# Performance work log

Hardware: AMD Instinct MI355X
Metric: run time of the kernel (lower is better)

The kernel has to match this reference:

```python
import jax, jax.numpy as jnp
import numpy as np

EPS = 1e-6
B = 4194304


def setup_inputs() -> dict:
    key = jax.random.key(0)
    k1, k2 = jax.random.split(key)
    ypred = jax.random.normal(k1, (B, 3, 3), dtype=jnp.float32)
    ytrue = jax.random.normal(k2, (B, 3, 3), dtype=jnp.float32)
    return {"ypred": ypred, "ytrue": ytrue}


def reference(ypred, ytrue):
    # trace(A^T B) == sum(A * B) elementwise -> one fused reduce per sample
    tr = jnp.sum(ypred * ytrue, axis=(1, 2))  # [B]
    cos = jnp.clip((tr - 1.0) * 0.5, -1.0 + EPS, 1.0 - EPS)
    angle = jnp.arccos(cos)
    return jnp.mean(angle)
```

## Files before the change

### kernel.cpp

```cpp
#include <hip/hip_runtime.h>


constexpr int TPB  = 256;
constexpr int NBLK = 2048;
constexpr float EPSF = 1e-6f;

__device__ __forceinline__ double block_reduce(double v) {
    __shared__ double sm[TPB / 64];
    const int lane = threadIdx.x & 63;
    const int wid  = threadIdx.x >> 6;
    #pragma unroll
    for (int off = 32; off > 0; off >>= 1) v += __shfl_down(v, off, 64);
    if (lane == 0) sm[wid] = v;
    __syncthreads();
    if (wid == 0) {
        v = (lane < TPB / 64) ? sm[lane] : 0.0;
        #pragma unroll
        for (int off = (TPB / 64) / 2; off > 0; off >>= 1) v += __shfl_down(v, off, 64);
    }
    return v;
}

__global__ __launch_bounds__(TPB) void geo_partial(
    const float* __restrict__ a, const float* __restrict__ b,
    double* __restrict__ partial, int nsamp)
{
    const long long tid    = (long long)blockIdx.x * TPB + threadIdx.x;
    const long long stride = (long long)gridDim.x * TPB;
    double acc = 0.0;

    for (long long g = tid; g * 4 < nsamp; g += stride) {
        const long long s0 = g * 4;
        const float4* pa = reinterpret_cast<const float4*>(a + s0 * 9);
        const float4* pb = reinterpret_cast<const float4*>(b + s0 * 9);

        float va[36], vb[36];
        #pragma unroll
        for (int j = 0; j < 9; ++j) {
            float4 x = pa[j];
            va[4*j+0] = x.x; va[4*j+1] = x.y; va[4*j+2] = x.z; va[4*j+3] = x.w;
        }
        #pragma unroll
        for (int j = 0; j < 9; ++j) {
            float4 y = pb[j];
            vb[4*j+0] = y.x; vb[4*j+1] = y.y; vb[4*j+2] = y.z; vb[4*j+3] = y.w;
        }

        #pragma unroll
        for (int k = 0; k < 4; ++k) {
            if (s0 + k < nsamp) {
                float dot = 0.0f;
                #pragma unroll
                for (int j = 0; j < 9; ++j) dot = fmaf(va[9*k+j], vb[9*k+j], dot);
                float c = (dot - 1.0f) * 0.5f;
                c = fminf(fmaxf(c, -1.0f + EPSF), 1.0f - EPSF);
                acc += (double)acosf(c);
            }
        }
    }

    double r = block_reduce(acc);
    if (threadIdx.x == 0) partial[blockIdx.x] = r;
}

__global__ __launch_bounds__(TPB) void geo_final(
    const double* __restrict__ partial, float* __restrict__ out,
    int n, double inv_n)
{
    double acc = 0.0;
    for (int i = threadIdx.x; i < n; i += TPB) acc += partial[i];
    double r = block_reduce(acc);
    if (threadIdx.x == 0) out[0] = (float)(r * inv_n);
}

extern "C" void kernel_launch(void* const* d_in, const int* in_sizes, int n_in,
                              void* d_out, int out_size, void* d_ws, size_t ws_size,
                              hipStream_t stream) {
    const float* a = (const float*)d_in[0];
    const float* b = (const float*)d_in[1];
    float* out = (float*)d_out;
    const int nsamp = in_sizes[0] / 9;

    double* partial = (double*)d_ws;

    geo_partial<<<NBLK, TPB, 0, stream>>>(a, b, partial, nsamp);
    geo_final<<<1, TPB, 0, stream>>>(partial, out, NBLK, 1.0 / (double)nsamp);
}
```

Before: 314.9 us.

## Load float4s coalesced per wave and assemble 3x3 dot products via lane shuffles

Each wave now reads 63 consecutive float4s from each input, covering 28 samples, so every lane does one coalesced load instead of nine strided float4 loads per thread. Each lane computes partial sums of its four products, and two cross-lane shuffles assemble each sample's 9-element dot product on an owner lane. This removes the uncoalesced access pattern and the large per-thread register arrays. The cost is extra shuffle and select logic, one idle lane per wave, and only 4 of 9 lanes computing acos, which lowers utilisation of the math units.

Result: faster. 308.6 us (-2.0%).

```diff
diff --git a/kernel.cpp b/kernel.cpp
--- a/kernel.cpp
+++ b/kernel.cpp
@@ -25,33 +25,46 @@
     const float* __restrict__ a, const float* __restrict__ b,
     double* __restrict__ partial, int nsamp)
 {
-    const long long tid    = (long long)blockIdx.x * TPB + threadIdx.x;
-    const long long stride = (long long)gridDim.x * TPB;
+    const int lane = threadIdx.x & 63;
+    const int wid  = threadIdx.x >> 6;
+    const long long gwave  = (long long)blockIdx.x * (TPB / 64) + wid;
+    const long long nwaves = (long long)gridDim.x * (TPB / 64);
+
+    const int g = lane / 9;
+    const int r = lane - 9 * g;
+    const bool active = (lane < 63);
+    const int head = (4 * r) / 9;
+    int nh = 9 * (head + 1) - 4 * r;
+    if (nh > 4) nh = 4;
+    const bool owner = active && ((r & 1) == 0) && (r < 8);
+    const int k = r >> 1;
+
+    const long long total_f4 = (long long)nsamp * 9 / 4;
+    const long long n_iters  = ((long long)nsamp + 27) / 28;
+
+    const float4* a4 = reinterpret_cast<const float4*>(a);
+    const float4* b4 = reinterpret_cast<const float4*>(b);
+
     double acc = 0.0;
+    for (long long it = gwave; it < n_iters; it += nwaves) {
+        const long long f4i = it * 63 + lane;
+        float4 x = make_float4(0.f, 0.f, 0.f, 0.f);
+        float4 y = make_float4(0.f, 0.f, 0.f, 0.f);
+        if (active && f4i < total_f4) { x = a4[f4i]; y = b4[f4i]; }
 
-    for (long long g = tid; g * 4 < nsamp; g += stride) {
-        const long long s0 = g * 4;
-        const float4* pa = reinterpret_cast<const float4*>(a + s0 * 9);
-        const float4* pb = reinterpret_cast<const float4*>(b + s0 * 9);
+        const float p0 = x.x * y.x, p1 = x.y * y.y, p2 = x.z * y.z, p3 = x.w * y.w;
+        const float pre2 = p0 + p1, pre3 = pre2 + p2, pre4 = pre3 + p3;
+        const float suf3 = p3, suf2 = p2 + p3, suf1 = p1 + suf2;
+        const float pearly = (nh == 1) ? p0 : (nh == 2) ? pre2 : (nh == 3) ? pre3 : pre4;
+        const float plate  = (nh == 4) ? pre4 : (nh == 1) ? suf1 : (nh == 2) ? suf2 : suf3;
 
-        float va[36], vb[36];
-        #pragma unroll
-        for (int j = 0; j < 9; ++j) {
-            float4 x = pa[j];
-            va[4*j+0] = x.x; va[4*j+1] = x.y; va[4*j+2] = x.z; va[4*j+3] = x.w;
-        }
-        #pragma unroll
-        for (int j = 0; j < 9; ++j) {
-            float4 y = pb[j];
-            vb[4*j+0] = y.x; vb[4*j+1] = y.y; vb[4*j+2] = y.z; vb[4*j+3] = y.w;
-        }
+        const float v1 = __shfl(plate,  lane + 1, 64);
+        const float v2 = __shfl(pearly, lane + 2, 64);
 
-        #pragma unroll
-        for (int k = 0; k < 4; ++k) {
-            if (s0 + k < nsamp) {
-                float dot = 0.0f;
-                #pragma unroll
-                for (int j = 0; j < 9; ++j) dot = fmaf(va[9*k+j], vb[9*k+j], dot);
+        if (owner) {
+            const long long s = it * 28 + 4 * g + k;
+            if (s < nsamp) {
+                const float dot = plate + v1 + v2;
                 float c = (dot - 1.0f) * 0.5f;
                 c = fminf(fmaxf(c, -1.0f + EPSF), 1.0f - EPSF);
                 acc += (double)acosf(c);
@@ -59,8 +72,8 @@
         }
     }
 
-    double r = block_reduce(acc);
-    if (threadIdx.x == 0) partial[blockIdx.x] = r;
+    const double rsum = block_reduce(acc);
+    if (threadIdx.x == 0) partial[blockIdx.x] = rsum;
 }
 
 __global__ __launch_bounds__(TPB) void geo_final(
@@ -69,7 +82,7 @@
 {
     double acc = 0.0;
     for (int i = threadIdx.x; i < n; i += TPB) acc += partial[i];
-    double r = block_reduce(acc);
+    const double r = block_reduce(acc);
     if (threadIdx.x == 0) out[0] = (float)(r * inv_n);
 }
 
```

## Stage sample tiles into LDS via double-buffered direct global-to-LDS loads

Applied to the files above, without the earlier changes.

Replaces per-thread strided float4 loads of 4 samples (144-byte stride, poorly coalesced) with wave-cooperative, fully coalesced global_load_lds transfers into double-buffered shared-memory tiles of 256 samples. Each thread then reads its 9 floats from LDS with an odd stride, which avoids bank conflicts. Manual vmcnt waits and barriers overlap the next tile's load with the current tile's compute. The grid is fixed at 1024 blocks × 16 tiles and has no grid-stride fallback, so it assumes the sample count is covered exactly.

Result: no change. 309.2 us (-1.8%).

```diff
diff --git a/kernel.cpp b/kernel.cpp
--- a/kernel.cpp
+++ b/kernel.cpp
@@ -1,9 +1,19 @@
 #include <hip/hip_runtime.h>
 
 
-constexpr int TPB  = 256;
-constexpr int NBLK = 2048;
+constexpr int TPB           = 256;
+constexpr int NBLK          = 1024;
+constexpr int SAMP_PER_TILE = 256;
+constexpr int TILE_F4       = SAMP_PER_TILE * 9 / 4;
+constexpr int TILES_PER_BLK = 16;
 constexpr float EPSF = 1e-6f;
+
+__device__ __forceinline__ void gload16_lds(const float4* g, float4* lds_base_uniform) {
+    __builtin_amdgcn_global_load_lds(
+        (const __attribute__((address_space(1))) void*)g,
+        (__attribute__((address_space(3))) void*)lds_base_uniform,
+        16, 0, 0);
+}
 
 __device__ __forceinline__ double block_reduce(double v) {
     __shared__ double sm[TPB / 64];
@@ -23,43 +33,60 @@
 
 __global__ __launch_bounds__(TPB) void geo_partial(
     const float* __restrict__ a, const float* __restrict__ b,
-    double* __restrict__ partial, int nsamp)
+    double* __restrict__ partial, long long nsamp)
 {
-    const long long tid    = (long long)blockIdx.x * TPB + threadIdx.x;
-    const long long stride = (long long)gridDim.x * TPB;
+    __shared__ float4 sA[2][TILE_F4];
+    __shared__ float4 sB[2][TILE_F4];
+
+    const int tid  = threadIdx.x;
+    const int lane = tid & 63;
+    const int wid  = tid >> 6;
+    const float4* a4 = reinterpret_cast<const float4*>(a);
+    const float4* b4 = reinterpret_cast<const float4*>(b);
+    const long long tile0 = (long long)blockIdx.x * TILES_PER_BLK;
+
+    auto stage = [&](int t, int bufsel) {
+        const long long base = (tile0 + t) * TILE_F4;
+        for (int i = wid; i < 18; i += 4) {
+            const int c = i >> 1;
+            if (i & 1) gload16_lds(b4 + base + c * 64 + lane, &sB[bufsel][c * 64]);
+            else       gload16_lds(a4 + base + c * 64 + lane, &sA[bufsel][c * 64]);
+        }
+    };
+
+    stage(0, 0);
     double acc = 0.0;
 
-    for (long long g = tid; g * 4 < nsamp; g += stride) {
-        const long long s0 = g * 4;
-        const float4* pa = reinterpret_cast<const float4*>(a + s0 * 9);
-        const float4* pb = reinterpret_cast<const float4*>(b + s0 * 9);
+    for (int t = 0; t < TILES_PER_BLK; ++t) {
+        const int cur = t & 1;
+        if (t + 1 < TILES_PER_BLK) {
+            stage(t + 1, cur ^ 1);
+            if (wid < 2) asm volatile("s_waitcnt vmcnt(5)" ::: "memory");
+            else         asm volatile("s_waitcnt vmcnt(4)" ::: "memory");
+        } else {
+            asm volatile("s_waitcnt vmcnt(0)" ::: "memory");
+        }
+        __builtin_amdgcn_s_barrier();
+        __builtin_amdgcn_sched_barrier(0);
 
-        float va[36], vb[36];
+        const float* pa = reinterpret_cast<const float*>(&sA[cur][0]) + 9 * tid;
+        const float* pb = reinterpret_cast<const float*>(&sB[cur][0]) + 9 * tid;
+        float dot = 0.0f;
         #pragma unroll
-        for (int j = 0; j < 9; ++j) {
-            float4 x = pa[j];
-            va[4*j+0] = x.x; va[4*j+1] = x.y; va[4*j+2] = x.z; va[4*j+3] = x.w;
-        }
-        #pragma unroll
-        for (int j = 0; j < 9; ++j) {
-            float4 y = pb[j];
-            vb[4*j+0] = y.x; vb[4*j+1] = y.y; vb[4*j+2] = y.z; vb[4*j+3] = y.w;
+        for (int j = 0; j < 9; ++j) dot = fmaf(pa[j], pb[j], dot);
+
+        const long long s = (tile0 + t) * SAMP_PER_TILE + tid;
+        if (s < nsamp) {
+            float c = (dot - 1.0f) * 0.5f;
+            c = fminf(fmaxf(c, -1.0f + EPSF), 1.0f - EPSF);
+            acc += (double)acosf(c);
         }
 
-        #pragma unroll
-        for (int k = 0; k < 4; ++k) {
-            if (s0 + k < nsamp) {
-                float dot = 0.0f;
-                #pragma unroll
-                for (int j = 0; j < 9; ++j) dot = fmaf(va[9*k+j], vb[9*k+j], dot);
-                float c = (dot - 1.0f) * 0.5f;
-                c = fminf(fmaxf(c, -1.0f + EPSF), 1.0f - EPSF);
-                acc += (double)acosf(c);
-            }
-        }
+        __builtin_amdgcn_sched_barrier(0);
+        __builtin_amdgcn_s_barrier();
     }
 
-    double r = block_reduce(acc);
+    const double r = block_reduce(acc);
     if (threadIdx.x == 0) partial[blockIdx.x] = r;
 }
 
@@ -69,7 +96,7 @@
 {
     double acc = 0.0;
     for (int i = threadIdx.x; i < n; i += TPB) acc += partial[i];
-    double r = block_reduce(acc);
+    const double r = block_reduce(acc);
     if (threadIdx.x == 0) out[0] = (float)(r * inv_n);
 }
 
@@ -79,7 +106,7 @@
     const float* a = (const float*)d_in[0];
     const float* b = (const float*)d_in[1];
     float* out = (float*)d_out;
-    const int nsamp = in_sizes[0] / 9;
+    const long long nsamp = in_sizes[0] / 9;
 
     double* partial = (double*)d_ws;
 
```
